# Kernel optimization log

Measured on AMD Instinct MI355X. Metric: run time of the kernel, lower is better.

Reference implementation:

```python
import jax, jax.numpy as jnp
import numpy as np

B, C, H, W, K = 16, 256, 32, 32, 8192


def setup_inputs() -> dict:
    key = jax.random.key(0)
    kx, kc = jax.random.split(key)
    x = jax.random.normal(kx, (B, C, H, W), dtype=jnp.float32)
    codebook = jax.random.normal(kc, (K, C), dtype=jnp.float32)
    return {"x": x, "codebook": codebook}


def reference(x, codebook):
    # x: [B, C, H, W], codebook: [K, C]
    b, c, h, w = x.shape
    xf = jnp.transpose(x, (0, 2, 3, 1)).reshape(-1, c)          # [N, C] tokens
    d = (jnp.sum(xf * xf, axis=1, keepdims=True)
         - 2.0 * (xf @ codebook.T)
         + jnp.sum(codebook * codebook, axis=1))
    idx = jnp.argmin(d, axis=1)                                  # [N] int
    q = codebook[idx]                                            # [N, C] gather
    # commitment loss (codebook side uses EMA, hence stop_gradient on q)
    commit_loss = jnp.mean((xf - jax.lax.stop_gradient(q)) ** 2)
    # straight-through estimator
    qf = xf + jax.lax.stop_gradient(q - xf)
    qe = jnp.transpose(qf.reshape(b, h, w, c), (0, 3, 1, 2))     # back to NCHW
    indices = idx.reshape(b, h, w)
    return qe, commit_loss, indices
```

## Files before the change

kernel.cpp:

```cpp
#include <hip/hip_runtime.h>
#include <hip/hip_bf16.h>
#include <stdint.h>

#define KK   8192
#define NN   16384
#define CCH  256

#define QE_SIZE  4194304
#define LOSS_OFF QE_SIZE
#define IDX_OFF  (QE_SIZE + 1)

#define B2_OFF     0ULL
#define HN_OFF     (B2_OFF + 8192ULL*256*2)
#define PK1_OFF    (HN_OFF + 8192ULL*4)
#define PK2_OFF    (PK1_OFF + 4ULL*16384*4)

typedef __attribute__((ext_vector_type(8))) short   bf16x8;
typedef __attribute__((ext_vector_type(8))) unsigned short ushort8v;
typedef __attribute__((ext_vector_type(4))) float   f32x4;

__device__ __forceinline__ void gld16(const void* g, void* l) {
    __builtin_amdgcn_global_load_lds(
        (const __attribute__((address_space(1))) void*)g,
        (__attribute__((address_space(3))) void*)l, 16, 0, 0);
}

__device__ __forceinline__ unsigned short bf16_rn(float v) {
    uint32_t u = __float_as_uint(v);
    return (unsigned short)((u + 0x7fffu + ((u >> 16) & 1u)) >> 16);
}

__device__ __forceinline__ void top3k_insert(unsigned& s1, int& i1,
                                             unsigned& s2, int& i2,
                                             unsigned& s3, int& i3,
                                             unsigned k, int g) {
    if (k > s1 || (k == s1 && g < i1)) {
        s3 = s2; i3 = i2; s2 = s1; i2 = i1; s1 = k; i1 = g;
    } else if (k > s2 || (k == s2 && g < i2)) {
        s3 = s2; i3 = i2; s2 = k; i2 = g;
    } else if (k > s3 || (k == s3 && g < i3)) {
        s3 = k; i3 = g;
    }
}

__global__ __launch_bounds__(256) void prep_kernel(const float* __restrict__ x,
                                                   const float* __restrict__ cb,
                                                   unsigned short* __restrict__ A,
                                                   unsigned short* __restrict__ B2,
                                                   float* __restrict__ hn,
                                                   float* __restrict__ loss) {
    __shared__ float xt[256 * 64];
    const int t = threadIdx.x;
    const int bid = blockIdx.x;

    if (bid >= 256) {
        const int cbid = bid - 256;
        if (cbid == 0 && t == 0) *loss = 0.f;
        const int code = cbid * 8 + (t >> 5);
        const int c8 = (t & 31) * 8;
        const float* cr = cb + (size_t)code * CCH + c8;
        float s = 0.f;
        unsigned short hi[8];
        #pragma unroll
        for (int u = 0; u < 8; ++u) {
            float v = cr[u];
            s += v * v;
            hi[u] = bf16_rn(v);
        }
        *(ushort8v*)(B2 + (size_t)code * 256 + c8) = *(ushort8v*)hi;
        #pragma unroll
        for (int off = 16; off; off >>= 1) s += __shfl_xor(s, off);
        if ((t & 31) == 0) hn[code] = -(0.5f * s + 256.0f);
        return;
    }

    const int n0 = bid * 64;
    const int b = n0 >> 10, hw0 = n0 & 1023;
    const int tok_l = t & 63, cg = t >> 6;
    const float* xb = x + ((size_t)b << 18) + hw0 + tok_l;
    #pragma unroll 8
    for (int i = 0; i < 64; ++i) {
        const int c = cg * 64 + i;
        xt[c * 64 + (tok_l ^ ((c >> 3) & 31))] = xb[(size_t)c << 10];
    }
    __syncthreads();
    const int tokq = t >> 5;
    const int c8 = (t & 31) * 8;
    const int sw = (c8 >> 3) & 31;
    const int ksh = c8 >> 5;
    const int lq  = (c8 >> 3) & 3;
    for (int p = 0; p < 8; ++p) {
        int tk = p * 8 + tokq;
        const int tks = tk ^ sw;
        unsigned short hi[8];
        #pragma unroll
        for (int u = 0; u < 8; ++u)
            hi[u] = bf16_rn(xt[(c8 + u) * 64 + tks]);
        const int n  = n0 + tk;
        const int tb = n >> 4;
        const int l  = (tk & 15) + 16 * lq;
        *(ushort8v*)(A + ((size_t)((tb * 8 + ksh) * 64) + l) * 8) = *(ushort8v*)hi;
    }
}

__global__ __launch_bounds__(256, 2) void vq_gemm_kernel(const unsigned short* __restrict__ A,
                                                         const unsigned short* __restrict__ B2,
                                                         const float* __restrict__ hn,
                                                         unsigned* __restrict__ pk1,
                                                         unsigned* __restrict__ pk2) {
    __shared__ unsigned short Bsm[2][4][4096];
    __shared__ float hn_sm[2048];

    const int t = threadIdx.x;
    const int lane = t & 63, wave = t >> 6;
    const int l15 = lane & 15, quad = lane >> 4;

    const int mblk = blockIdx.x & 127;
    const int nq   = blockIdx.x >> 7;
    const int codeQ = nq * 2048;

    bf16x8 af[2][8];
    #pragma unroll
    for (int i = 0; i < 2; ++i) {
        const int tb = mblk * 8 + wave * 2 + i;
        const unsigned short* Abase = A + ((size_t)(tb * 8) * 64 + lane) * 8;
        #pragma unroll
        for (int ks = 0; ks < 8; ++ks)
            af[i][ks] = *(const bf16x8*)(Abase + (size_t)ks * 64 * 8);
    }

    #pragma unroll
    for (int i = 0; i < 2; ++i) {
        const int boff = (wave * 2 + i) * 1024;
        gld16((const char*)(hn + codeQ) + boff + lane * 16,
              (char*)hn_sm + boff);
    }

    const int srow = wave * 8 + (lane >> 3);
    const int sch  = (lane & 7) ^ (srow & 7);

#define STAGE_NT(P, NT)                                                        \
    do {                                                                       \
        _Pragma("unroll")                                                      \
        for (int s_ = 0; s_ < 4; ++s_) {                                       \
            char* dst = (char*)Bsm[P][s_] + wave * 1024;                       \
            const size_t bOff = (size_t)(codeQ + (NT) * 64 + srow) * 256       \
                                + s_ * 64 + sch * 8;                           \
            _Pragma("unroll")                                                  \
            for (int it = 0; it < 2; ++it)                                     \
                gld16(B2 + bOff + (size_t)it * (32 * 256), dst + it * 4096);   \
        }                                                                      \
    } while (0)

    unsigned K1[2][4], K2[2][4];
    #pragma unroll
    for (int i = 0; i < 2; ++i)
        #pragma unroll
        for (int r = 0; r < 4; ++r) { K1[i][r] = 0u; K2[i][r] = 0u; }

    STAGE_NT(0, 0);
    __syncthreads();

    #pragma unroll 1
    for (int nt = 0; nt < 32; ++nt) {
        if (nt + 1 < 32) STAGE_NT((nt + 1) & 1, nt + 1);

        const int hb = nt * 64 + l15;
        f32x4 acc[2][4];
        #pragma unroll
        for (int j = 0; j < 4; ++j) {
            const float nh = hn_sm[hb + j * 16];
            #pragma unroll
            for (int i = 0; i < 2; ++i) {
                f32x4 z = {nh, nh, nh, nh};
                acc[i][j] = z;
            }
        }

        #pragma unroll
        for (int st = 0; st < 4; ++st) {
            const char* bs = (const char*)Bsm[nt & 1][st];
            #pragma unroll
            for (int ks2 = 0; ks2 < 2; ++ks2) {
                bf16x8 bfr[4];
                #pragma unroll
                for (int j = 0; j < 4; ++j) {
                    const int rowB = j * 16 + l15;
                    const int cbk = ((quad ^ (rowB & 7)) ^ (ks2 << 2)) * 16;
                    bfr[j] = *(const bf16x8*)(bs + rowB * 128 + cbk);
                }
                const int ka = st * 2 + ks2;
                #pragma unroll
                for (int i = 0; i < 2; ++i)
                    #pragma unroll
                    for (int j = 0; j < 4; ++j)
                        acc[i][j] = __builtin_amdgcn_mfma_f32_16x16x32_bf16(
                            af[i][ka], bfr[j], acc[i][j], 0, 0, 0);
            }
        }

        const int icb = 2047 - (nt * 64 + l15);
        #pragma unroll
        for (int j = 0; j < 4; ++j) {
            const unsigned ic = (unsigned)(icb - j * 16);
            #pragma unroll
            for (int i = 0; i < 2; ++i)
                #pragma unroll
                for (int r = 0; r < 4; ++r) {
                    const unsigned u = __float_as_uint(acc[i][j][r]);
                    const unsigned k = (~u & 0xFFFFF800u) | ic;
                    const unsigned lo = min(k, K1[i][r]);
                    K1[i][r] = max(k, K1[i][r]);
                    K2[i][r] = max(K2[i][r], lo);
                }
        }

        __syncthreads();
    }
#undef STAGE_NT

    #pragma unroll
    for (int off = 1; off < 16; off <<= 1) {
        #pragma unroll
        for (int i = 0; i < 2; ++i)
            #pragma unroll
            for (int r = 0; r < 4; ++r) {
                const unsigned t1 = __shfl_xor(K1[i][r], off);
                const unsigned t2 = __shfl_xor(K2[i][r], off);
                const unsigned lo = min(K1[i][r], t1);
                K1[i][r] = max(K1[i][r], t1);
                K2[i][r] = max(max(K2[i][r], t2), lo);
            }
    }

    if (l15 == 0) {
        #pragma unroll
        for (int i = 0; i < 2; ++i)
            #pragma unroll
            for (int r = 0; r < 4; ++r) {
                const int tok = mblk * 128 + wave * 32 + i * 16 + quad * 4 + r;
                const int gi = nq * NN + tok;
                pk1[gi] = K1[i][r]; pk2[gi] = K2[i][r];
            }
    }
}

__global__ __launch_bounds__(512) void finalize_kernel(const float* __restrict__ x,
                                                       const float* __restrict__ cb,
                                                       const unsigned* __restrict__ pk1,
                                                       const unsigned* __restrict__ pk2,
                                                       float* __restrict__ qe,
                                                       float* __restrict__ idx_f,
                                                       float* __restrict__ loss) {
    __shared__ float  xt[256 * 65];
    __shared__ int    cnd[3][64], bsx[64];
    __shared__ double dp[3][8][64];

    const int t = threadIdx.x;
    const int n0 = blockIdx.x * 64;
    const int b = n0 >> 10, hw0 = n0 & 1023;
    const int tok_l = t & 63, cg = t >> 6;

    if (t < 64) {
        unsigned s1 = 0u, s2 = 0u, s3 = 0u;
        int i1 = 0x7ffffff, i2 = 0x7ffffff, i3 = 0x7ffffff;
        const int n = n0 + t;
        #pragma unroll
        for (int q = 0; q < 4; ++q) {
            const unsigned ka = pk1[q * NN + n];
            const unsigned kb = pk2[q * NN + n];
            const int ga = q * 2048 + 2047 - (int)(ka & 2047u);
            const int gb = q * 2048 + 2047 - (int)(kb & 2047u);
            top3k_insert(s1, i1, s2, i2, s3, i3, ka, ga);
            top3k_insert(s1, i1, s2, i2, s3, i3, kb, gb);
        }
        cnd[0][t] = i1; cnd[1][t] = i2; cnd[2][t] = i3;
    }

    const float* xb = x + ((size_t)b << 18) + hw0 + tok_l;
    #pragma unroll 8
    for (int i = 0; i < 32; ++i) {
        const int c = cg * 32 + i;
        xt[c * 65 + tok_l] = xb[(size_t)c << 10];
    }
    __syncthreads();

    {
        const int tok = t & 63, cq = t >> 6;
        const float* c0 = cb + (size_t)cnd[0][tok] * CCH + cq * 32;
        const float* c1 = cb + (size_t)cnd[1][tok] * CCH + cq * 32;
        const float* c2 = cb + (size_t)cnd[2][tok] * CCH + cq * 32;
        double d0 = 0.0, d1 = 0.0, d2 = 0.0;
        #pragma unroll
        for (int j = 0; j < 32; j += 4) {
            const f32x4 e0 = *(const f32x4*)(c0 + j);
            const f32x4 e1 = *(const f32x4*)(c1 + j);
            const f32x4 e2 = *(const f32x4*)(c2 + j);
            #pragma unroll
            for (int u = 0; u < 4; ++u) {
                const float xv = xt[(cq * 32 + j + u) * 65 + tok];
                const double dx0 = (double)xv - (double)e0[u];
                const double dx1 = (double)xv - (double)e1[u];
                const double dx2 = (double)xv - (double)e2[u];
                d0 += dx0 * dx0;
                d1 += dx1 * dx1;
                d2 += dx2 * dx2;
            }
        }
        dp[0][cq][tok] = d0; dp[1][cq][tok] = d1; dp[2][cq][tok] = d2;
    }
    __syncthreads();

    if (t < 64) {
        double dd[3]; int ii[3];
        #pragma unroll
        for (int c = 0; c < 3; ++c) {
            double s = 0.0;
            #pragma unroll
            for (int q = 0; q < 8; ++q) s += dp[c][q][t];
            dd[c] = s;
            ii[c] = cnd[c][t];
        }
        int bi = ii[0]; double bd = dd[0];
        if (dd[1] < bd || (dd[1] == bd && ii[1] < bi)) { bd = dd[1]; bi = ii[1]; }
        if (dd[2] < bd || (dd[2] == bd && ii[2] < bi)) { bd = dd[2]; bi = ii[2]; }
        bsx[t] = bi;
        idx_f[n0 + t] = (float)bi;
        float lsum = (float)bd;
        #pragma unroll
        for (int off = 32; off; off >>= 1) lsum += __shfl_down(lsum, off);
        if (t == 0) atomicAdd(loss, lsum * (1.0f / ((float)NN * (float)CCH)));
    }
    __syncthreads();

    {
        const int w = t >> 6, lane = t & 63;
        #pragma unroll
        for (int i = 0; i < 8; ++i) {
            const int tok = w * 8 + i;
            const float* e = cb + (size_t)bsx[tok] * CCH;
            #pragma unroll
            for (int u = 0; u < 4; ++u) {
                const int c = u * 64 + lane;
                xt[c * 65 + tok] = e[c];
            }
        }
    }
    __syncthreads();

    float* qb = qe + ((size_t)b << 18) + hw0 + tok_l;
    #pragma unroll 8
    for (int i = 0; i < 32; ++i) {
        const int c = cg * 32 + i;
        qb[(size_t)c << 10] = xt[c * 65 + tok_l];
    }
}

extern "C" void kernel_launch(void* const* d_in, const int* in_sizes, int n_in,
                              void* d_out, int out_size, void* d_ws, size_t ws_size,
                              hipStream_t stream) {
    const float* x  = (const float*)d_in[0];
    const float* cb = (const float*)d_in[1];
    float* out = (float*)d_out;
    char* ws = (char*)d_ws;

    unsigned short* A  = (unsigned short*)out;
    unsigned short* B2 = (unsigned short*)(ws + B2_OFF);
    float* hn  = (float*)(ws + HN_OFF);
    unsigned* pk1 = (unsigned*)(ws + PK1_OFF);
    unsigned* pk2 = (unsigned*)(ws + PK2_OFF);

    prep_kernel    <<<256 + KK / 8, 256, 0, stream>>>(x, cb, A, B2, hn,
                                                      out + LOSS_OFF);
    vq_gemm_kernel <<<512, 256, 0, stream>>>(A, B2, hn, pk1, pk2);
    finalize_kernel<<<NN / 64, 512, 0, stream>>>(x, cb, pk1, pk2,
                                                 out, out + IDX_OFF,
                                                 out + LOSS_OFF);
}
```

Before: 165.1 us.

## Pre-layout codebook in MFMA fragment order and read B directly from global

The prep kernel now writes the bf16 codebook in a tiled order that matches the MFMA B-fragment lane layout. The GEMM kernel therefore loads B fragments straight from global memory and drops the LDS double-buffer staging and the per-tile barriers. The aim is to remove LDS traffic and synchronisation. In exchange, all four waves fetch the same B data on their own, which puts more pressure on L1/L2 and leaves no explicit prefetch to hide load latency. Separately, the finalize kernel is reworked to handle 32 tokens per 256-thread block, with an XOR-swizzled transpose buffer in place of padding, giving more and smaller blocks.

Result: slower. 230.2 us (+39.5%).

```diff
diff --git a/kernel.cpp b/kernel.cpp
--- a/kernel.cpp
+++ b/kernel.cpp
@@ -67,7 +67,9 @@
             s += v * v;
             hi[u] = bf16_rn(v);
         }
-        *(ushort8v*)(B2 + (size_t)code * 256 + c8) = *(ushort8v*)hi;
+        const int ct = code >> 4, ksh = c8 >> 5, lq = (c8 >> 3) & 3;
+        *(ushort8v*)(B2 + ((size_t)((ct * 8 + ksh) * 64) + lq * 16 + (code & 15)) * 8)
+            = *(ushort8v*)hi;
         #pragma unroll
         for (int off = 16; off; off >>= 1) s += __shfl_xor(s, off);
         if ((t & 31) == 0) hn[code] = -(0.5f * s + 256.0f);
@@ -108,12 +110,11 @@
                                                          const float* __restrict__ hn,
                                                          unsigned* __restrict__ pk1,
                                                          unsigned* __restrict__ pk2) {
-    __shared__ unsigned short Bsm[2][4][4096];
     __shared__ float hn_sm[2048];
 
     const int t = threadIdx.x;
     const int lane = t & 63, wave = t >> 6;
-    const int l15 = lane & 15, quad = lane >> 4;
+    const int l15 = lane & 15;
 
     const int mblk = blockIdx.x & 127;
     const int nq   = blockIdx.x >> 7;
@@ -135,22 +136,9 @@
         gld16((const char*)(hn + codeQ) + boff + lane * 16,
               (char*)hn_sm + boff);
     }
-
-    const int srow = wave * 8 + (lane >> 3);
-    const int sch  = (lane & 7) ^ (srow & 7);
-
-#define STAGE_NT(P, NT)                                                        \
-    do {                                                                       \
-        _Pragma("unroll")                                                      \
-        for (int s_ = 0; s_ < 4; ++s_) {                                       \
-            char* dst = (char*)Bsm[P][s_] + wave * 1024;                       \
-            const size_t bOff = (size_t)(codeQ + (NT) * 64 + srow) * 256       \
-                                + s_ * 64 + sch * 8;                           \
-            _Pragma("unroll")                                                  \
-            for (int it = 0; it < 2; ++it)                                     \
-                gld16(B2 + bOff + (size_t)it * (32 * 256), dst + it * 4096);   \
-        }                                                                      \
-    } while (0)
+    __syncthreads();
+
+    const char* Bq = (const char*)B2 + (size_t)(nq * 128) * 8192 + lane * 16;
 
     unsigned K1[2][4], K2[2][4];
     #pragma unroll
@@ -158,12 +146,9 @@
         #pragma unroll
         for (int r = 0; r < 4; ++r) { K1[i][r] = 0u; K2[i][r] = 0u; }
 
-    STAGE_NT(0, 0);
-    __syncthreads();
-
     #pragma unroll 1
     for (int nt = 0; nt < 32; ++nt) {
-        if (nt + 1 < 32) STAGE_NT((nt + 1) & 1, nt + 1);
+        const char* Bt = Bq + (size_t)nt * 32768;
 
         const int hb = nt * 64 + l15;
         f32x4 acc[2][4];
@@ -178,25 +163,17 @@
         }
 
         #pragma unroll
-        for (int st = 0; st < 4; ++st) {
-            const char* bs = (const char*)Bsm[nt & 1][st];
-            #pragma unroll
-            for (int ks2 = 0; ks2 < 2; ++ks2) {
-                bf16x8 bfr[4];
+        for (int ka = 0; ka < 8; ++ka) {
+            bf16x8 bfr[4];
+            #pragma unroll
+            for (int j = 0; j < 4; ++j)
+                bfr[j] = *(const bf16x8*)(Bt + j * 8192 + ka * 1024);
+            #pragma unroll
+            for (int i = 0; i < 2; ++i)
                 #pragma unroll
-                for (int j = 0; j < 4; ++j) {
-                    const int rowB = j * 16 + l15;
-                    const int cbk = ((quad ^ (rowB & 7)) ^ (ks2 << 2)) * 16;
-                    bfr[j] = *(const bf16x8*)(bs + rowB * 128 + cbk);
-                }
-                const int ka = st * 2 + ks2;
-                #pragma unroll
-                for (int i = 0; i < 2; ++i)
-                    #pragma unroll
-                    for (int j = 0; j < 4; ++j)
-                        acc[i][j] = __builtin_amdgcn_mfma_f32_16x16x32_bf16(
-                            af[i][ka], bfr[j], acc[i][j], 0, 0, 0);
-            }
+                for (int j = 0; j < 4; ++j)
+                    acc[i][j] = __builtin_amdgcn_mfma_f32_16x16x32_bf16(
+                        af[i][ka], bfr[j], acc[i][j], 0, 0, 0);
         }
 
         const int icb = 2047 - (nt * 64 + l15);
@@ -214,10 +191,7 @@
                     K2[i][r] = max(K2[i][r], lo);
                 }
         }
-
-        __syncthreads();
-    }
-#undef STAGE_NT
+    }
 
     #pragma unroll
     for (int off = 1; off < 16; off <<= 1) {
@@ -234,6 +208,7 @@
     }
 
     if (l15 == 0) {
+        const int quad = lane >> 4;
         #pragma unroll
         for (int i = 0; i < 2; ++i)
             #pragma unroll
@@ -245,23 +220,23 @@
     }
 }
 
-__global__ __launch_bounds__(512) void finalize_kernel(const float* __restrict__ x,
+__global__ __launch_bounds__(256) void finalize_kernel(const float* __restrict__ x,
                                                        const float* __restrict__ cb,
                                                        const unsigned* __restrict__ pk1,
                                                        const unsigned* __restrict__ pk2,
                                                        float* __restrict__ qe,
                                                        float* __restrict__ idx_f,
                                                        float* __restrict__ loss) {
-    __shared__ float  xt[256 * 65];
-    __shared__ int    cnd[3][64], bsx[64];
-    __shared__ double dp[3][8][64];
+    __shared__ float  xt[256 * 32];
+    __shared__ int    cnd[3][32], bsx[32];
+    __shared__ double dp[3][8][32];
 
     const int t = threadIdx.x;
-    const int n0 = blockIdx.x * 64;
+    const int n0 = blockIdx.x * 32;
     const int b = n0 >> 10, hw0 = n0 & 1023;
-    const int tok_l = t & 63, cg = t >> 6;
-
-    if (t < 64) {
+    const int tok_l = t & 31, cg = t >> 5;
+
+    if (t < 32) {
         unsigned s1 = 0u, s2 = 0u, s3 = 0u;
         int i1 = 0x7ffffff, i2 = 0x7ffffff, i3 = 0x7ffffff;
         const int n = n0 + t;
@@ -281,12 +256,12 @@
     #pragma unroll 8
     for (int i = 0; i < 32; ++i) {
         const int c = cg * 32 + i;
-        xt[c * 65 + tok_l] = xb[(size_t)c << 10];
+        xt[c * 32 + (tok_l ^ (c & 31))] = xb[(size_t)c << 10];
     }
     __syncthreads();
 
     {
-        const int tok = t & 63, cq = t >> 6;
+        const int tok = t & 31, cq = t >> 5;
         const float* c0 = cb + (size_t)cnd[0][tok] * CCH + cq * 32;
         const float* c1 = cb + (size_t)cnd[1][tok] * CCH + cq * 32;
         const float* c2 = cb + (size_t)cnd[2][tok] * CCH + cq * 32;
@@ -298,7 +273,8 @@
             const f32x4 e2 = *(const f32x4*)(c2 + j);
             #pragma unroll
             for (int u = 0; u < 4; ++u) {
-                const float xv = xt[(cq * 32 + j + u) * 65 + tok];
+                const int c = cq * 32 + j + u;
+                const float xv = xt[c * 32 + (tok ^ (c & 31))];
                 const double dx0 = (double)xv - (double)e0[u];
                 const double dx1 = (double)xv - (double)e1[u];
                 const double dx2 = (double)xv - (double)e2[u];
@@ -311,7 +287,7 @@
     }
     __syncthreads();
 
-    if (t < 64) {
+    if (t < 32) {
         double dd[3]; int ii[3];
         #pragma unroll
         for (int c = 0; c < 3; ++c) {
@@ -328,7 +304,7 @@
         idx_f[n0 + t] = (float)bi;
         float lsum = (float)bd;
         #pragma unroll
-        for (int off = 32; off; off >>= 1) lsum += __shfl_down(lsum, off);
+        for (int off = 16; off; off >>= 1) lsum += __shfl_down(lsum, off);
         if (t == 0) atomicAdd(loss, lsum * (1.0f / ((float)NN * (float)CCH)));
     }
     __syncthreads();
@@ -342,7 +318,7 @@
             #pragma unroll
             for (int u = 0; u < 4; ++u) {
                 const int c = u * 64 + lane;
-                xt[c * 65 + tok] = e[c];
+                xt[c * 32 + (tok ^ (c & 31))] = e[c];
             }
         }
     }
@@ -352,7 +328,7 @@
     #pragma unroll 8
     for (int i = 0; i < 32; ++i) {
         const int c = cg * 32 + i;
-        qb[(size_t)c << 10] = xt[c * 65 + tok_l];
+        qb[(size_t)c << 10] = xt[c * 32 + (tok_l ^ (c & 31))];
     }
 }
 
@@ -373,7 +349,7 @@
     prep_kernel    <<<256 + KK / 8, 256, 0, stream>>>(x, cb, A, B2, hn,
                                                       out + LOSS_OFF);
     vq_gemm_kernel <<<512, 256, 0, stream>>>(A, B2, hn, pk1, pk2);
-    finalize_kernel<<<NN / 64, 512, 0, stream>>>(x, cb, pk1, pk2,
+    finalize_kernel<<<NN / 32, 256, 0, stream>>>(x, cb, pk1, pk2,
                                                  out, out + IDX_OFF,
                                                  out + LOSS_OFF);
 }
```

## Fuse prep, GEMM and finalize into one cooperative kernel with grid syncs

Applied to the files above, without the earlier changes.

Merges the three launches into a single cooperative kernel of 512 blocks. Grid-wide barriers separate the prep, distance-GEMM/top-2 and finalize phases, and shared memory is reused across the phases. Finalize is redistributed so each block handles 32 tokens instead of 64, with an XOR-swizzled transpose buffer. The aim is to remove kernel launch gaps and tail effects, at the cost of grid.sync overhead and a prep phase that uses fewer blocks. If the cooperative launch fails, it falls back to the original three kernels.

After: 445.7 us. 170% more time.

```diff
diff --git a/kernel.cpp b/kernel.cpp
--- a/kernel.cpp
+++ b/kernel.cpp
@@ -1,6 +1,9 @@
 #include <hip/hip_runtime.h>
+#include <hip/hip_cooperative_groups.h>
 #include <hip/hip_bf16.h>
 #include <stdint.h>
+
+namespace cg = cooperative_groups;
 
 #define KK   8192
 #define NN   16384
@@ -43,101 +46,101 @@
     }
 }
 
-__global__ __launch_bounds__(256) void prep_kernel(const float* __restrict__ x,
-                                                   const float* __restrict__ cb,
-                                                   unsigned short* __restrict__ A,
-                                                   unsigned short* __restrict__ B2,
-                                                   float* __restrict__ hn,
-                                                   float* __restrict__ loss) {
-    __shared__ float xt[256 * 64];
+__global__ __launch_bounds__(256, 2) void vq_fused_kernel(
+        const float* __restrict__ x, const float* __restrict__ cb,
+        unsigned short* __restrict__ A, unsigned short* __restrict__ B2,
+        float* __restrict__ hn, unsigned* __restrict__ pk1,
+        unsigned* __restrict__ pk2, float* __restrict__ qe,
+        float* __restrict__ idx_f, float* __restrict__ loss) {
+    __shared__ __align__(16) char smem[73728];
     const int t = threadIdx.x;
     const int bid = blockIdx.x;
-
-    if (bid >= 256) {
-        const int cbid = bid - 256;
-        if (cbid == 0 && t == 0) *loss = 0.f;
-        const int code = cbid * 8 + (t >> 5);
+    cg::grid_group grid = cg::this_grid();
+
+    if (bid < 256) {
+        float* xt = (float*)smem;
+        const int n0 = bid * 64;
+        const int b = n0 >> 10, hw0 = n0 & 1023;
+        const int tok_l = t & 63, cg_ = t >> 6;
+        const float* xb = x + ((size_t)b << 18) + hw0 + tok_l;
+        #pragma unroll 8
+        for (int i = 0; i < 64; ++i) {
+            const int c = cg_ * 64 + i;
+            xt[c * 64 + (tok_l ^ ((c >> 3) & 31))] = xb[(size_t)c << 10];
+        }
+        __syncthreads();
+        const int tokq = t >> 5;
         const int c8 = (t & 31) * 8;
-        const float* cr = cb + (size_t)code * CCH + c8;
-        float s = 0.f;
-        unsigned short hi[8];
-        #pragma unroll
-        for (int u = 0; u < 8; ++u) {
-            float v = cr[u];
-            s += v * v;
-            hi[u] = bf16_rn(v);
-        }
-        *(ushort8v*)(B2 + (size_t)code * 256 + c8) = *(ushort8v*)hi;
-        #pragma unroll
-        for (int off = 16; off; off >>= 1) s += __shfl_xor(s, off);
-        if ((t & 31) == 0) hn[code] = -(0.5f * s + 256.0f);
-        return;
-    }
-
-    const int n0 = bid * 64;
-    const int b = n0 >> 10, hw0 = n0 & 1023;
-    const int tok_l = t & 63, cg = t >> 6;
-    const float* xb = x + ((size_t)b << 18) + hw0 + tok_l;
-    #pragma unroll 8
-    for (int i = 0; i < 64; ++i) {
-        const int c = cg * 64 + i;
-        xt[c * 64 + (tok_l ^ ((c >> 3) & 31))] = xb[(size_t)c << 10];
-    }
-    __syncthreads();
-    const int tokq = t >> 5;
-    const int c8 = (t & 31) * 8;
-    const int sw = (c8 >> 3) & 31;
-    const int ksh = c8 >> 5;
-    const int lq  = (c8 >> 3) & 3;
-    for (int p = 0; p < 8; ++p) {
-        int tk = p * 8 + tokq;
-        const int tks = tk ^ sw;
-        unsigned short hi[8];
-        #pragma unroll
-        for (int u = 0; u < 8; ++u)
-            hi[u] = bf16_rn(xt[(c8 + u) * 64 + tks]);
-        const int n  = n0 + tk;
-        const int tb = n >> 4;
-        const int l  = (tk & 15) + 16 * lq;
-        *(ushort8v*)(A + ((size_t)((tb * 8 + ksh) * 64) + l) * 8) = *(ushort8v*)hi;
-    }
-}
-
-__global__ __launch_bounds__(256, 2) void vq_gemm_kernel(const unsigned short* __restrict__ A,
-                                                         const unsigned short* __restrict__ B2,
-                                                         const float* __restrict__ hn,
-                                                         unsigned* __restrict__ pk1,
-                                                         unsigned* __restrict__ pk2) {
-    __shared__ unsigned short Bsm[2][4][4096];
-    __shared__ float hn_sm[2048];
-
-    const int t = threadIdx.x;
-    const int lane = t & 63, wave = t >> 6;
-    const int l15 = lane & 15, quad = lane >> 4;
-
-    const int mblk = blockIdx.x & 127;
-    const int nq   = blockIdx.x >> 7;
-    const int codeQ = nq * 2048;
-
-    bf16x8 af[2][8];
-    #pragma unroll
-    for (int i = 0; i < 2; ++i) {
-        const int tb = mblk * 8 + wave * 2 + i;
-        const unsigned short* Abase = A + ((size_t)(tb * 8) * 64 + lane) * 8;
-        #pragma unroll
-        for (int ks = 0; ks < 8; ++ks)
-            af[i][ks] = *(const bf16x8*)(Abase + (size_t)ks * 64 * 8);
-    }
-
-    #pragma unroll
-    for (int i = 0; i < 2; ++i) {
-        const int boff = (wave * 2 + i) * 1024;
-        gld16((const char*)(hn + codeQ) + boff + lane * 16,
-              (char*)hn_sm + boff);
-    }
-
-    const int srow = wave * 8 + (lane >> 3);
-    const int sch  = (lane & 7) ^ (srow & 7);
+        const int sw = (c8 >> 3) & 31;
+        const int ksh = c8 >> 5;
+        const int lq  = (c8 >> 3) & 3;
+        for (int p = 0; p < 8; ++p) {
+            int tk = p * 8 + tokq;
+            const int tks = tk ^ sw;
+            unsigned short hi[8];
+            #pragma unroll
+            for (int u = 0; u < 8; ++u)
+                hi[u] = bf16_rn(xt[(c8 + u) * 64 + tks]);
+            const int n  = n0 + tk;
+            const int tb = n >> 4;
+            const int l  = (tk & 15) + 16 * lq;
+            *(ushort8v*)(A + ((size_t)((tb * 8 + ksh) * 64) + l) * 8) = *(ushort8v*)hi;
+        }
+    } else {
+        if (bid == 256 && t == 0) *loss = 0.f;
+        for (int g = 0; g < 4; ++g) {
+            const int cbid = (bid - 256) * 4 + g;
+            const int code = cbid * 8 + (t >> 5);
+            const int c8 = (t & 31) * 8;
+            const float* cr = cb + (size_t)code * CCH + c8;
+            float s = 0.f;
+            unsigned short hi[8];
+            #pragma unroll
+            for (int u = 0; u < 8; ++u) {
+                float v = cr[u];
+                s += v * v;
+                hi[u] = bf16_rn(v);
+            }
+            *(ushort8v*)(B2 + (size_t)code * 256 + c8) = *(ushort8v*)hi;
+            #pragma unroll
+            for (int off = 16; off; off >>= 1) s += __shfl_xor(s, off);
+            if ((t & 31) == 0) hn[code] = -(0.5f * s + 256.0f);
+        }
+    }
+
+    __threadfence();
+    grid.sync();
+    __threadfence();
+
+    {
+        unsigned short (*Bsm)[4][4096] = (unsigned short (*)[4][4096])smem;
+        float* hn_sm = (float*)(smem + 65536);
+
+        const int lane = t & 63, wave = t >> 6;
+        const int l15 = lane & 15, quad = lane >> 4;
+        const int mblk = bid & 127;
+        const int nq   = bid >> 7;
+        const int codeQ = nq * 2048;
+
+        bf16x8 af[2][8];
+        #pragma unroll
+        for (int i = 0; i < 2; ++i) {
+            const int tb = mblk * 8 + wave * 2 + i;
+            const unsigned short* Abase = A + ((size_t)(tb * 8) * 64 + lane) * 8;
+            #pragma unroll
+            for (int ks = 0; ks < 8; ++ks)
+                af[i][ks] = *(const bf16x8*)(Abase + (size_t)ks * 64 * 8);
+        }
+
+        #pragma unroll
+        for (int i = 0; i < 2; ++i) {
+            const int boff = (wave * 2 + i) * 1024;
+            gld16((const char*)(hn + codeQ) + boff + lane * 16,
+                  (char*)hn_sm + boff);
+        }
+
+        const int srow = wave * 8 + (lane >> 3);
+        const int sch  = (lane & 7) ^ (srow & 7);
 
 #define STAGE_NT(P, NT)                                                        \
     do {                                                                       \
@@ -152,6 +155,321 @@
         }                                                                      \
     } while (0)
 
+        unsigned K1[2][4], K2[2][4];
+        #pragma unroll
+        for (int i = 0; i < 2; ++i)
+            #pragma unroll
+            for (int r = 0; r < 4; ++r) { K1[i][r] = 0u; K2[i][r] = 0u; }
+
+        STAGE_NT(0, 0);
+        __syncthreads();
+
+        #pragma unroll 1
+        for (int nt = 0; nt < 32; ++nt) {
+            if (nt + 1 < 32) STAGE_NT((nt + 1) & 1, nt + 1);
+
+            const int hb = nt * 64 + l15;
+            f32x4 acc[2][4];
+            #pragma unroll
+            for (int j = 0; j < 4; ++j) {
+                const float nh = hn_sm[hb + j * 16];
+                #pragma unroll
+                for (int i = 0; i < 2; ++i) {
+                    f32x4 z = {nh, nh, nh, nh};
+                    acc[i][j] = z;
+                }
+            }
+
+            #pragma unroll
+            for (int st = 0; st < 4; ++st) {
+                const char* bs = (const char*)Bsm[nt & 1][st];
+                #pragma unroll
+                for (int ks2 = 0; ks2 < 2; ++ks2) {
+                    bf16x8 bfr[4];
+                    #pragma unroll
+                    for (int j = 0; j < 4; ++j) {
+                        const int rowB = j * 16 + l15;
+                        const int cbk = ((quad ^ (rowB & 7)) ^ (ks2 << 2)) * 16;
+                        bfr[j] = *(const bf16x8*)(bs + rowB * 128 + cbk);
+                    }
+                    const int ka = st * 2 + ks2;
+                    #pragma unroll
+                    for (int i = 0; i < 2; ++i)
+                        #pragma unroll
+                        for (int j = 0; j < 4; ++j)
+                            acc[i][j] = __builtin_amdgcn_mfma_f32_16x16x32_bf16(
+                                af[i][ka], bfr[j], acc[i][j], 0, 0, 0);
+                }
+            }
+
+            const int icb = 2047 - (nt * 64 + l15);
+            #pragma unroll
+            for (int j = 0; j < 4; ++j) {
+                const unsigned ic = (unsigned)(icb - j * 16);
+                #pragma unroll
+                for (int i = 0; i < 2; ++i)
+                    #pragma unroll
+                    for (int r = 0; r < 4; ++r) {
+                        const unsigned u = __float_as_uint(acc[i][j][r]);
+                        const unsigned k = (~u & 0xFFFFF800u) | ic;
+                        const unsigned lo = min(k, K1[i][r]);
+                        K1[i][r] = max(k, K1[i][r]);
+                        K2[i][r] = max(K2[i][r], lo);
+                    }
+            }
+
+            __syncthreads();
+        }
+#undef STAGE_NT
+
+        #pragma unroll
+        for (int off = 1; off < 16; off <<= 1) {
+            #pragma unroll
+            for (int i = 0; i < 2; ++i)
+                #pragma unroll
+                for (int r = 0; r < 4; ++r) {
+                    const unsigned t1 = __shfl_xor(K1[i][r], off);
+                    const unsigned t2 = __shfl_xor(K2[i][r], off);
+                    const unsigned lo = min(K1[i][r], t1);
+                    K1[i][r] = max(K1[i][r], t1);
+                    K2[i][r] = max(max(K2[i][r], t2), lo);
+                }
+        }
+
+        if (l15 == 0) {
+            #pragma unroll
+            for (int i = 0; i < 2; ++i)
+                #pragma unroll
+                for (int r = 0; r < 4; ++r) {
+                    const int tok = mblk * 128 + wave * 32 + i * 16 + quad * 4 + r;
+                    const int gi = nq * NN + tok;
+                    pk1[gi] = K1[i][r]; pk2[gi] = K2[i][r];
+                }
+        }
+    }
+
+    __threadfence();
+    grid.sync();
+    __threadfence();
+
+    {
+        float*  xt  = (float*)smem;
+        int*    cnd = (int*)(smem + 32768);
+        int*    bsx = (int*)(smem + 32768 + 384);
+        double* dp  = (double*)(smem + 32768 + 512);
+
+        const int n0 = bid * 32;
+        const int b = n0 >> 10, hw0 = n0 & 1023;
+        const int tok_l = t & 31, cg_ = t >> 5;
+
+        if (t < 32) {
+            unsigned s1 = 0u, s2 = 0u, s3 = 0u;
+            int i1 = 0x7ffffff, i2 = 0x7ffffff, i3 = 0x7ffffff;
+            const int n = n0 + t;
+            #pragma unroll
+            for (int q = 0; q < 4; ++q) {
+                const unsigned ka = pk1[q * NN + n];
+                const unsigned kb = pk2[q * NN + n];
+                const int ga = q * 2048 + 2047 - (int)(ka & 2047u);
+                const int gb = q * 2048 + 2047 - (int)(kb & 2047u);
+                top3k_insert(s1, i1, s2, i2, s3, i3, ka, ga);
+                top3k_insert(s1, i1, s2, i2, s3, i3, kb, gb);
+            }
+            cnd[t] = i1; cnd[32 + t] = i2; cnd[64 + t] = i3;
+        }
+
+        const float* xb = x + ((size_t)b << 18) + hw0 + tok_l;
+        #pragma unroll 8
+        for (int i = 0; i < 32; ++i) {
+            const int c = cg_ * 32 + i;
+            xt[c * 32 + (tok_l ^ (c & 31))] = xb[(size_t)c << 10];
+        }
+        __syncthreads();
+
+        {
+            const int tok = t & 31, cq = t >> 5;
+            const float* c0 = cb + (size_t)cnd[tok]      * CCH + cq * 32;
+            const float* c1 = cb + (size_t)cnd[32 + tok] * CCH + cq * 32;
+            const float* c2 = cb + (size_t)cnd[64 + tok] * CCH + cq * 32;
+            double d0 = 0.0, d1 = 0.0, d2 = 0.0;
+            #pragma unroll
+            for (int j = 0; j < 32; j += 4) {
+                const f32x4 e0 = *(const f32x4*)(c0 + j);
+                const f32x4 e1 = *(const f32x4*)(c1 + j);
+                const f32x4 e2 = *(const f32x4*)(c2 + j);
+                #pragma unroll
+                for (int u = 0; u < 4; ++u) {
+                    const int c = cq * 32 + j + u;
+                    const float xv = xt[c * 32 + (tok ^ (c & 31))];
+                    const double dx0 = (double)xv - (double)e0[u];
+                    const double dx1 = (double)xv - (double)e1[u];
+                    const double dx2 = (double)xv - (double)e2[u];
+                    d0 += dx0 * dx0;
+                    d1 += dx1 * dx1;
+                    d2 += dx2 * dx2;
+                }
+            }
+            dp[(0 * 8 + cq) * 32 + tok] = d0;
+            dp[(1 * 8 + cq) * 32 + tok] = d1;
+            dp[(2 * 8 + cq) * 32 + tok] = d2;
+        }
+        __syncthreads();
+
+        if (t < 32) {
+            double dd[3]; int ii[3];
+            #pragma unroll
+            for (int c = 0; c < 3; ++c) {
+                double s = 0.0;
+                #pragma unroll
+                for (int q = 0; q < 8; ++q) s += dp[(c * 8 + q) * 32 + t];
+                dd[c] = s;
+                ii[c] = cnd[c * 32 + t];
+            }
+            int bi = ii[0]; double bd = dd[0];
+            if (dd[1] < bd || (dd[1] == bd && ii[1] < bi)) { bd = dd[1]; bi = ii[1]; }
+            if (dd[2] < bd || (dd[2] == bd && ii[2] < bi)) { bd = dd[2]; bi = ii[2]; }
+            bsx[t] = bi;
+            idx_f[n0 + t] = (float)bi;
+            float lsum = (float)bd;
+            #pragma unroll
+            for (int off = 16; off; off >>= 1) lsum += __shfl_down(lsum, off);
+            if (t == 0) atomicAdd(loss, lsum * (1.0f / ((float)NN * (float)CCH)));
+        }
+        __syncthreads();
+
+        {
+            const int w = t >> 6, lane = t & 63;
+            #pragma unroll
+            for (int i = 0; i < 8; ++i) {
+                const int tok = w * 8 + i;
+                const float* e = cb + (size_t)bsx[tok] * CCH;
+                #pragma unroll
+                for (int u = 0; u < 4; ++u) {
+                    const int c = u * 64 + lane;
+                    xt[c * 32 + (tok ^ (c & 31))] = e[c];
+                }
+            }
+        }
+        __syncthreads();
+
+        float* qb = qe + ((size_t)b << 18) + hw0 + tok_l;
+        #pragma unroll 8
+        for (int i = 0; i < 32; ++i) {
+            const int c = cg_ * 32 + i;
+            qb[(size_t)c << 10] = xt[c * 32 + (tok_l ^ (c & 31))];
+        }
+    }
+}
+
+__global__ __launch_bounds__(256) void prep_kernel(const float* __restrict__ x,
+                                                   const float* __restrict__ cb,
+                                                   unsigned short* __restrict__ A,
+                                                   unsigned short* __restrict__ B2,
+                                                   float* __restrict__ hn,
+                                                   float* __restrict__ loss) {
+    __shared__ float xt[256 * 64];
+    const int t = threadIdx.x;
+    const int bid = blockIdx.x;
+
+    if (bid >= 256) {
+        const int cbid = bid - 256;
+        if (cbid == 0 && t == 0) *loss = 0.f;
+        const int code = cbid * 8 + (t >> 5);
+        const int c8 = (t & 31) * 8;
+        const float* cr = cb + (size_t)code * CCH + c8;
+        float s = 0.f;
+        unsigned short hi[8];
+        #pragma unroll
+        for (int u = 0; u < 8; ++u) {
+            float v = cr[u];
+            s += v * v;
+            hi[u] = bf16_rn(v);
+        }
+        *(ushort8v*)(B2 + (size_t)code * 256 + c8) = *(ushort8v*)hi;
+        #pragma unroll
+        for (int off = 16; off; off >>= 1) s += __shfl_xor(s, off);
+        if ((t & 31) == 0) hn[code] = -(0.5f * s + 256.0f);
+        return;
+    }
+
+    const int n0 = bid * 64;
+    const int b = n0 >> 10, hw0 = n0 & 1023;
+    const int tok_l = t & 63, cg_ = t >> 6;
+    const float* xb = x + ((size_t)b << 18) + hw0 + tok_l;
+    #pragma unroll 8
+    for (int i = 0; i < 64; ++i) {
+        const int c = cg_ * 64 + i;
+        xt[c * 64 + (tok_l ^ ((c >> 3) & 31))] = xb[(size_t)c << 10];
+    }
+    __syncthreads();
+    const int tokq = t >> 5;
+    const int c8 = (t & 31) * 8;
+    const int sw = (c8 >> 3) & 31;
+    const int ksh = c8 >> 5;
+    const int lq  = (c8 >> 3) & 3;
+    for (int p = 0; p < 8; ++p) {
+        int tk = p * 8 + tokq;
+        const int tks = tk ^ sw;
+        unsigned short hi[8];
+        #pragma unroll
+        for (int u = 0; u < 8; ++u)
+            hi[u] = bf16_rn(xt[(c8 + u) * 64 + tks]);
+        const int n  = n0 + tk;
+        const int tb = n >> 4;
+        const int l  = (tk & 15) + 16 * lq;
+        *(ushort8v*)(A + ((size_t)((tb * 8 + ksh) * 64) + l) * 8) = *(ushort8v*)hi;
+    }
+}
+
+__global__ __launch_bounds__(256, 2) void vq_gemm_kernel(const unsigned short* __restrict__ A,
+                                                         const unsigned short* __restrict__ B2,
+                                                         const float* __restrict__ hn,
+                                                         unsigned* __restrict__ pk1,
+                                                         unsigned* __restrict__ pk2) {
+    __shared__ unsigned short Bsm[2][4][4096];
+    __shared__ float hn_sm[2048];
+
+    const int t = threadIdx.x;
+    const int lane = t & 63, wave = t >> 6;
+    const int l15 = lane & 15, quad = lane >> 4;
+
+    const int mblk = blockIdx.x & 127;
+    const int nq   = blockIdx.x >> 7;
+    const int codeQ = nq * 2048;
+
+    bf16x8 af[2][8];
+    #pragma unroll
+    for (int i = 0; i < 2; ++i) {
+        const int tb = mblk * 8 + wave * 2 + i;
+        const unsigned short* Abase = A + ((size_t)(tb * 8) * 64 + lane) * 8;
+        #pragma unroll
+        for (int ks = 0; ks < 8; ++ks)
+            af[i][ks] = *(const bf16x8*)(Abase + (size_t)ks * 64 * 8);
+    }
+
+    #pragma unroll
+    for (int i = 0; i < 2; ++i) {
+        const int boff = (wave * 2 + i) * 1024;
+        gld16((const char*)(hn + codeQ) + boff + lane * 16,
+              (char*)hn_sm + boff);
+    }
+
+    const int srow = wave * 8 + (lane >> 3);
+    const int sch  = (lane & 7) ^ (srow & 7);
+
+#define STAGE_NT(P, NT)                                                        \
+    do {                                                                       \
+        _Pragma("unroll")                                                      \
+        for (int s_ = 0; s_ < 4; ++s_) {                                       \
+            char* dst = (char*)Bsm[P][s_] + wave * 1024;                       \
+            const size_t bOff = (size_t)(codeQ + (NT) * 64 + srow) * 256       \
+                                + s_ * 64 + sch * 8;                           \
+            _Pragma("unroll")                                                  \
+            for (int it = 0; it < 2; ++it)                                     \
+                gld16(B2 + bOff + (size_t)it * (32 * 256), dst + it * 4096);   \
+        }                                                                      \
+    } while (0)
+
     unsigned K1[2][4], K2[2][4];
     #pragma unroll
     for (int i = 0; i < 2; ++i)
@@ -259,7 +577,7 @@
     const int t = threadIdx.x;
     const int n0 = blockIdx.x * 64;
     const int b = n0 >> 10, hw0 = n0 & 1023;
-    const int tok_l = t & 63, cg = t >> 6;
+    const int tok_l = t & 63, cg_ = t >> 6;
 
     if (t < 64) {
         unsigned s1 = 0u, s2 = 0u, s3 = 0u;
@@ -280,7 +598,7 @@
     const float* xb = x + ((size_t)b << 18) + hw0 + tok_l;
     #pragma unroll 8
     for (int i = 0; i < 32; ++i) {
-        const int c = cg * 32 + i;
+        const int c = cg_ * 32 + i;
         xt[c * 65 + tok_l] = xb[(size_t)c << 10];
     }
     __syncthreads();
@@ -351,7 +669,7 @@
     float* qb = qe + ((size_t)b << 18) + hw0 + tok_l;
     #pragma unroll 8
     for (int i = 0; i < 32; ++i) {
-        const int c = cg * 32 + i;
+        const int c = cg_ * 32 + i;
         qb[(size_t)c << 10] = xt[c * 65 + tok_l];
     }
 }
@@ -369,11 +687,21 @@
     float* hn  = (float*)(ws + HN_OFF);
     unsigned* pk1 = (unsigned*)(ws + PK1_OFF);
     unsigned* pk2 = (unsigned*)(ws + PK2_OFF);
-
-    prep_kernel    <<<256 + KK / 8, 256, 0, stream>>>(x, cb, A, B2, hn,
-                                                      out + LOSS_OFF);
-    vq_gemm_kernel <<<512, 256, 0, stream>>>(A, B2, hn, pk1, pk2);
-    finalize_kernel<<<NN / 64, 512, 0, stream>>>(x, cb, pk1, pk2,
-                                                 out, out + IDX_OFF,
-                                                 out + LOSS_OFF);
+    float* qe    = out;
+    float* idx_f = out + IDX_OFF;
+    float* loss  = out + LOSS_OFF;
+
+    void* args[] = {(void*)&x, (void*)&cb, (void*)&A, (void*)&B2, (void*)&hn,
+                    (void*)&pk1, (void*)&pk2, (void*)&qe, (void*)&idx_f,
+                    (void*)&loss};
+    hipError_t err = hipLaunchCooperativeKernel((const void*)vq_fused_kernel,
+                                                dim3(512), dim3(256), args, 0,
+                                                stream);
+    if (err != hipSuccess) {
+        (void)hipGetLastError();
+        prep_kernel    <<<256 + KK / 8, 256, 0, stream>>>(x, cb, A, B2, hn, loss);
+        vq_gemm_kernel <<<512, 256, 0, stream>>>(A, B2, hn, pk1, pk2);
+        finalize_kernel<<<NN / 64, 512, 0, stream>>>(x, cb, pk1, pk2,
+                                                     qe, idx_f, loss);
+    }
 }
```
